# Optimization experiments

Hardware: AMD Instinct MI355X
Metric: run time of the kernel (lower is better)

Reference implementation:

```python
import jax, jax.numpy as jnp
import numpy as np

B, S, N, C = 8, 256, 256, 64
NH = 8
H, W = 256, 256
D = N * C // NH  # per-head channel dim = 2048
EPS = 1e-12


def window_reverse(windows, ws, Hh, Ww, Cc):
    # windows: (B, S, N, C) -> (B, H*W, C)
    b = windows.shape[0]
    x = windows.reshape(b, Hh // ws[0], Ww // ws[1], ws[0], ws[1], Cc)
    x = x.transpose(0, 1, 3, 2, 4, 5).reshape(b, Hh, Ww, Cc).reshape(b, Hh * Ww, Cc)
    return x


def window_partition(x, ws):
    # x: (B, H, W, C) -> (B, nWin, winElems, C)
    b, hh, ww, cc = x.shape
    x = x.reshape(b, hh // ws[0], ws[0], ww // ws[1], ws[1], cc)
    return x.transpose(0, 1, 3, 2, 4, 5).reshape(b, (hh // ws[0]) * (ww // ws[1]), ws[0] * ws[1], cc)


def setup_inputs() -> dict:
    key = jax.random.key(0)
    ks = jax.random.split(key, 6)
    x = jax.random.normal(ks[0], (B, S, N, C), dtype=jnp.float32)
    qkv_w = jax.random.normal(ks[1], (4 * C, C), dtype=jnp.float32) * 0.02
    qkv_b = jnp.zeros((4 * C,), dtype=jnp.float32)
    proj_w = jax.random.normal(ks[2], (C, C), dtype=jnp.float32) * 0.02
    proj_b = jnp.zeros((C,), dtype=jnp.float32)
    temperature1 = jnp.ones((NH, 1, 1), dtype=jnp.float32)
    temperature2 = jnp.ones((NH, 1, 1), dtype=jnp.float32)
    return {"x": x, "qkv_w": qkv_w, "qkv_b": qkv_b, "proj_w": proj_w,
            "proj_b": proj_b, "temperature1": temperature1, "temperature2": temperature2}


def reference(x, qkv_w, qkv_b, proj_w, proj_b, temperature1, temperature2):
    b, s, n, c = x.shape
    xf = x.reshape(b, s * n, c)
    # fused 4-way qkv projection (q, k, v_H, v_V)
    qkvv = (xf @ qkv_w.T + qkv_b).reshape(b, s, 4, NH, D).transpose(2, 0, 3, 1, 4)
    q, k, v_H, v_V = qkvv[0], qkvv[1], qkvv[2], qkvv[3]  # each (B, NH, S, D)

    # reorient v_V from H-windows (columns) to V-windows (rows)
    v_V = v_V.transpose(0, 2, 1, 3).reshape(b, s, n, c)       # (B,S,N,C)
    v_V = v_V.transpose(0, 2, 1, 3)                           # (B,N,S,C)
    v_V = window_reverse(v_V, (H, 1), H, W, c).reshape(b, H, W, c)
    v_V = window_partition(v_V, (1, W))                       # (B,H,W,C)
    v_V = v_V.transpose(0, 2, 1, 3)                           # (B,W,H,C) == (B,S,N,C)
    v_V = v_V.reshape(b, s, NH, D).transpose(0, 2, 1, 3)      # (B,NH,S,D)

    # cosine attention over S with per-head temperature
    qn = q / jnp.maximum(jnp.linalg.norm(q, axis=-1, keepdims=True), EPS)
    kn = k / jnp.maximum(jnp.linalg.norm(k, axis=-1, keepdims=True), EPS)
    sim = jnp.einsum('bhsd,bhtd->bhst', qn, kn)  # (B,NH,S,S)
    attn_H = jax.nn.softmax(sim * temperature1, axis=-1)
    attn_V = jax.nn.softmax(sim * temperature2, axis=-1)

    x_H = jnp.einsum('bhst,bhtd->bhsd', attn_H, v_H).transpose(0, 2, 1, 3).reshape(b, s * n, c)
    x_V = jnp.einsum('bhst,bhtd->bhsd', attn_V, v_V).transpose(0, 2, 1, 3).reshape(b, s * n, c)

    out = (x_H + x_V) @ proj_w.T + proj_b
    return out.reshape(b, s, n, c)
```

## Files before the change

kernel.cpp:

```cpp
#include <hip/hip_runtime.h>


using half_t = _Float16;
using half8 = __attribute__((ext_vector_type(8))) _Float16;
using f32x4 = __attribute__((ext_vector_type(4))) float;

#define NTOK 524288

#define GLDS(g, l) __builtin_amdgcn_global_load_lds( \
    (const __attribute__((address_space(1))) void*)(g), \
    (__attribute__((address_space(3))) void*)(l), 16, 0, 0)

#define WS_Q      0
#define WS_K      67108864
#define WS_VH     134217728
#define WS_VV     201326592
#define WS_XHV    268435456
#define WS_NQ     335544320
#define WS_NK     335609856
#define WS_WH     335675392
#define WS_WP     335708160

__global__ void kW0(const float* __restrict__ qkv_w, const float* __restrict__ proj_w,
                    half_t* __restrict__ Wh, half_t* __restrict__ Wp) {
    int tid = threadIdx.x;
    for (int i = tid; i < 256 * 64; i += 256) Wh[i] = (half_t)qkv_w[i];
    for (int i = tid; i < 64 * 64; i += 256) Wp[i] = (half_t)proj_w[i];
}

__device__ inline void y_tile_mfma(const float* __restrict__ xb,
                                   const half_t* __restrict__ Wh,
                                   int tbase, int hi, int lo,
                                   f32x4 (&acc)[4][4], int wave, int lane) {
    const int l15 = lane & 15, quad = lane >> 4;
#pragma unroll
    for (int kc = 0; kc < 2; ++kc) {
        const int c = kc * 32 + quad * 8;
        half8 afr[4];
#pragma unroll
        for (int mt = 0; mt < 4; ++mt) {
            int m = mt * 16 + l15;
            int token = tbase + (m >> 3) * hi + (m & 7) * lo;
            const float* p = xb + (size_t)token * 64 + c;
            f32x4 f0 = *(const f32x4*)p;
            f32x4 f1 = *(const f32x4*)(p + 4);
            half8 a;
            a[0] = (half_t)f0[0]; a[1] = (half_t)f0[1]; a[2] = (half_t)f0[2]; a[3] = (half_t)f0[3];
            a[4] = (half_t)f1[0]; a[5] = (half_t)f1[1]; a[6] = (half_t)f1[2]; a[7] = (half_t)f1[3];
            afr[mt] = a;
        }
#pragma unroll
        for (int i = 0; i < 4; ++i) {
            int j = (wave * 4 + i) * 16 + l15;
            half8 bfr = *(const half8*)(Wh + j * 64 + c);
#pragma unroll
            for (int mt = 0; mt < 4; ++mt)
                acc[mt][i] = __builtin_amdgcn_mfma_f32_16x16x32_f16(afr[mt], bfr, acc[mt][i], 0, 0, 0);
        }
    }
}

__device__ inline void y_dump_rowmajor(f32x4 (&acc)[4][4], const float* __restrict__ qkv_b,
                                       half_t* ylds, int wave, int lane) {
    const int l15 = lane & 15, quad = lane >> 4;
#pragma unroll
    for (int i = 0; i < 4; ++i) {
        int j = (wave * 4 + i) * 16 + l15;
        float bj = qkv_b[j];
#pragma unroll
        for (int mt = 0; mt < 4; ++mt)
#pragma unroll
            for (int r = 0; r < 4; ++r)
                ylds[(mt * 16 + quad * 4 + r) * 264 + j] = (half_t)(acc[mt][i][r] + bj);
    }
}

__device__ inline void y_dump_transposed(f32x4 (&acc)[4][4], const float* __restrict__ qkv_b,
                                         half_t* yldsT, int wave, int lane) {
    const int l15 = lane & 15, quad = lane >> 4;
#pragma unroll
    for (int i = 0; i < 4; ++i) {
        int j = (wave * 4 + i) * 16 + l15;
        float bj = qkv_b[j];
#pragma unroll
        for (int mt = 0; mt < 4; ++mt)
#pragma unroll
            for (int r = 0; r < 4; ++r)
                yldsT[j * 72 + mt * 16 + quad * 4 + r] = (half_t)(acc[mt][i][r] + bj);
    }
}

__global__ __launch_bounds__(256) void kA1(const float* __restrict__ x,
                                           const half_t* __restrict__ Wh,
                                           const float* __restrict__ qkv_b,
                                           half_t* __restrict__ Q, half_t* __restrict__ K,
                                           float* __restrict__ normQ, float* __restrict__ normK) {
    __shared__ half_t ylds[64 * 264];
    __shared__ float scr[256];
    int idx = blockIdx.x;
    int sb = idx & 31; idx >>= 5;
    int h = idx & 7; idx >>= 3;
    int g = idx & 1; int b = idx >> 1;
    int s0 = sb * 8;
    int n0 = g * 64 + h * 8;
    int tid = threadIdx.x, wave = tid >> 6, lane = tid & 63;
    const float* xb = x + (size_t)b * 65536 * 64;
    f32x4 acc[4][4];
#pragma unroll
    for (int a = 0; a < 4; ++a)
#pragma unroll
        for (int c = 0; c < 4; ++c) acc[a][c] = {0.f, 0.f, 0.f, 0.f};
    y_tile_mfma(xb, Wh, s0 * 256 + n0, 256, 1, acc, wave, lane);
    y_dump_rowmajor(acc, qkv_b, ylds, wave, lane);
    __syncthreads();
    half_t* dst = (g == 0 ? Q : K) + ((size_t)(b * 8 + h) * 256 + s0) * 2048;
    int ns = tid >> 5, jc = (tid & 31) * 8;
#pragma unroll
    for (int si = 0; si < 8; ++si) {
        half8 v = *(const half8*)&ylds[(si * 8 + ns) * 264 + jc];
        *(half8*)(dst + (size_t)si * 2048 + ns * 256 + jc) = v;
    }
    float sum = 0.f;
#pragma unroll
    for (int nn = 0; nn < 8; ++nn) {
        half8 v = *(const half8*)&ylds[((tid >> 5) * 8 + nn) * 264 + (tid & 31) * 8];
#pragma unroll
        for (int e = 0; e < 8; ++e) { float f = (float)v[e]; sum += f * f; }
    }
    scr[tid] = sum;
    __syncthreads();
    if (tid < 8) {
        float s = 0.f;
        for (int k2 = 0; k2 < 32; ++k2) s += scr[tid * 32 + k2];
        float* nd = (g == 0 ? normQ : normK);
        nd[(b * 8 + h) * 256 + s0 + tid] = s;
    }
}

__global__ __launch_bounds__(256) void kA2H(const float* __restrict__ x,
                                            const half_t* __restrict__ Wh,
                                            const float* __restrict__ qkv_b,
                                            half_t* __restrict__ VH) {
    __shared__ half_t yldsT[256 * 72];
    int idx = blockIdx.x;
    int sb = idx & 3; idx >>= 2;
    int nn = idx & 63; int b = idx >> 6;
    int h = nn >> 3, ns = nn & 7;
    int n = 128 + nn;
    int s0 = sb * 64;
    int tid = threadIdx.x, wave = tid >> 6, lane = tid & 63;
    const float* xb = x + (size_t)b * 65536 * 64;
    f32x4 acc[4][4];
#pragma unroll
    for (int a = 0; a < 4; ++a)
#pragma unroll
        for (int c = 0; c < 4; ++c) acc[a][c] = {0.f, 0.f, 0.f, 0.f};
    y_tile_mfma(xb, Wh, s0 * 256 + n, 2048, 256, acc, wave, lane);
    y_dump_transposed(acc, qkv_b, yldsT, wave, lane);
    __syncthreads();
    int jl = lane >> 3, tc = lane & 7;
    half_t* base = VH + ((size_t)(b * 8 + h) * 2048 + ns * 256) * 256 + s0 + tc * 8;
#pragma unroll
    for (int u = 0; u < 8; ++u) {
        int j = wave * 64 + u * 8 + jl;
        half8 v = *(const half8*)&yldsT[j * 72 + tc * 8];
        *(half8*)(base + (size_t)j * 256) = v;
    }
}

__global__ __launch_bounds__(256) void kA2V(const float* __restrict__ x,
                                            const half_t* __restrict__ Wh,
                                            const float* __restrict__ qkv_b,
                                            half_t* __restrict__ VV) {
    __shared__ half_t vlds[64 * 264];
    int idx = blockIdx.x;
    int st = idx & 255; int b = idx >> 8;
    int h = st >> 5;
    int tid = threadIdx.x, wave = tid >> 6, lane = tid & 63;
    const float* xb = x + (size_t)b * 65536 * 64;
    f32x4 acc[4][4];
#pragma unroll
    for (int a = 0; a < 4; ++a)
#pragma unroll
        for (int c = 0; c < 4; ++c) acc[a][c] = {0.f, 0.f, 0.f, 0.f};
    y_tile_mfma(xb, Wh, st * 256 + 192, 8, 1, acc, wave, lane);
    {
        const int l15 = lane & 15, quad = lane >> 4;
#pragma unroll
        for (int i = 0; i < 4; ++i) {
            int j = (wave * 4 + i) * 16 + l15;
            float bj = qkv_b[j];
            int dm = j & 63;
            int jc = j >> 6;
#pragma unroll
            for (int mt = 0; mt < 4; ++mt)
#pragma unroll
                for (int r = 0; r < 4; ++r) {
                    int m = mt * 16 + quad * 4 + r;
                    int t = 32 * (m >> 3) + 4 * (m & 7) + jc;
                    vlds[dm * 264 + t] = (half_t)(acc[mt][i][r] + bj);
                }
        }
    }
    __syncthreads();
    half_t* base = VV + ((size_t)(b * 8 + h) * 2048 + (st & 31) * 64) * 256;
    int l31 = lane & 31, lh = lane >> 5;
#pragma unroll
    for (int u = 0; u < 8; ++u) {
        int dm = u * 8 + wave * 2 + lh;
        half8 v = *(const half8*)&vlds[dm * 264 + l31 * 8];
        *(half8*)(base + (size_t)dm * 256 + l31 * 8) = v;
    }
}

__global__ __launch_bounds__(1024, 4) void kB(const half_t* __restrict__ Q, const half_t* __restrict__ K,
                                              const half_t* __restrict__ VH, const half_t* __restrict__ VV,
                                              const float* __restrict__ normQ, const float* __restrict__ normK,
                                              const float* __restrict__ temp1, const float* __restrict__ temp2,
                                              half_t* __restrict__ xhv) {
    extern __shared__ char smem[];
    char* Ks0 = smem;
    char* Ks1 = smem + 32768;
    char* Qs0 = smem + 65536;
    char* Qs1 = smem + 73728;
    half_t* PH = (half_t*)(smem + 81920);
    half_t* PV = (half_t*)(smem + 115712);
    float* rq  = (float*)(smem + 149504);
    float* rk  = (float*)(smem + 149760);

    int idx = blockIdx.x;
    int bh = idx & 63;
    int sqb = idx >> 6;
    int h = bh & 7, b = bh >> 3;
    int sq0 = sqb * 64;
    int tid = threadIdx.x, wave = tid >> 6, lane = tid & 63;
    int l15 = lane & 15, quad = lane >> 4;
    float t1 = temp1[h], t2 = temp2[h];
    const half_t* Qb = Q + (size_t)bh * 256 * 2048;
    const half_t* Kb = K + (size_t)bh * 256 * 2048;
    const half_t* VHb = VH + (size_t)bh * 2048 * 256;
    const half_t* VVb = VV + (size_t)bh * 2048 * 256;

    if (tid < 64) rq[tid] = 1.f / fmaxf(sqrtf(normQ[bh * 256 + sq0 + tid]), 1e-12f);
    if (tid < 256) rk[tid] = 1.f / fmaxf(sqrtf(normK[bh * 256 + tid]), 1e-12f);

    {
        const int l7 = lane & 7, l8 = lane >> 3;
        const int swzh = (l7 ^ (l8 & 7)) * 8;
        const half_t* gK0 = Kb + (size_t)(wave * 8 + l8) * 2048 + swzh;
        const half_t* gK1 = Kb + (size_t)(128 + wave * 8 + l8) * 2048 + swzh;
        const half_t* gQ  = Qb + (size_t)(sq0 + (wave & 7) * 8 + l8) * 2048 + swzh;

        auto STAGE = [&](int kk, char* KsB, char* QsB) {
            const int off = kk * 64;
            GLDS(gK0 + off, KsB + wave * 1024);
            GLDS(gK1 + off, KsB + 16384 + wave * 1024);
            if (wave < 8) GLDS(gQ + off, QsB + wave * 1024);
        };

        f32x4 acc1[4];
#pragma unroll
        for (int a = 0; a < 4; ++a) acc1[a] = {0.f, 0.f, 0.f, 0.f};
        const int tcol = wave * 16 + l15;
        const int ts7 = tcol & 7;

        auto COMPUTE = [&](const char* KsB_, const char* QsB_) {
            const half_t* KsB = (const half_t*)KsB_;
            const half_t* QsB = (const half_t*)QsB_;
#pragma unroll
            for (int sub = 0; sub < 2; ++sub) {
                int c16 = sub * 4 + quad;
                half8 bfr = *(const half8*)(KsB + tcol * 64 + (c16 ^ ts7) * 8);
#pragma unroll
                for (int mt = 0; mt < 4; ++mt) {
                    int m = mt * 16 + l15;
                    half8 afr = *(const half8*)(QsB + m * 64 + (c16 ^ (m & 7)) * 8);
                    acc1[mt] = __builtin_amdgcn_mfma_f32_16x16x32_f16(afr, bfr, acc1[mt], 0, 0, 0);
                }
            }
        };

        STAGE(0, Ks0, Qs0);
        __syncthreads();
        for (int kk = 0; kk < 32; kk += 2) {
            if (kk + 1 < 32) STAGE(kk + 1, Ks1, Qs1);
            COMPUTE(Ks0, Qs0);
            __syncthreads();
            if (kk + 2 < 32) STAGE(kk + 2, Ks0, Qs0);
            COMPUTE(Ks1, Qs1);
            __syncthreads();
        }
        float rkt = rk[tcol];
#pragma unroll
        for (int mt = 0; mt < 4; ++mt)
#pragma unroll
            for (int r = 0; r < 4; ++r) {
                int row = mt * 16 + quad * 4 + r;
                PH[row * 264 + tcol] = (half_t)(acc1[mt][r] * rq[row] * rkt);
            }
    }
    __syncthreads();

    {
        int r_ = tid >> 4, cc = tid & 15;
        half_t* phrow = &PH[r_ * 264 + cc * 16];
        half_t* pvrow = &PV[r_ * 264 + cc * 16];
        half8 v0 = *(const half8*)phrow;
        half8 v1 = *(const half8*)(phrow + 8);
        float fv[16];
#pragma unroll
        for (int e = 0; e < 8; ++e) { fv[e] = (float)v0[e]; fv[8 + e] = (float)v1[e]; }
        float mx = fv[0], mn = fv[0];
#pragma unroll
        for (int e = 1; e < 16; ++e) { mx = fmaxf(mx, fv[e]); mn = fminf(mn, fv[e]); }
#pragma unroll
        for (int m = 1; m < 16; m <<= 1) {
            mx = fmaxf(mx, __shfl_xor(mx, m, 16));
            mn = fminf(mn, __shfl_xor(mn, m, 16));
        }
        float mh = (t1 >= 0.f) ? t1 * mx : t1 * mn;
        float mv = (t2 >= 0.f) ? t2 * mx : t2 * mn;
        float sh = 0.f, sv = 0.f;
#pragma unroll
        for (int e = 0; e < 16; ++e) {
            sh += __expf(fv[e] * t1 - mh);
            sv += __expf(fv[e] * t2 - mv);
        }
#pragma unroll
        for (int m = 1; m < 16; m <<= 1) {
            sh += __shfl_xor(sh, m, 16);
            sv += __shfl_xor(sv, m, 16);
        }
        float rh = 1.f / sh, rv = 1.f / sv;
        half8 o0, o1, p0, p1;
#pragma unroll
        for (int e = 0; e < 8; ++e) {
            o0[e] = (half_t)(__expf(fv[e] * t1 - mh) * rh);
            o1[e] = (half_t)(__expf(fv[8 + e] * t1 - mh) * rh);
            p0[e] = (half_t)(__expf(fv[e] * t2 - mv) * rv);
            p1[e] = (half_t)(__expf(fv[8 + e] * t2 - mv) * rv);
        }
        *(half8*)phrow = o0; *(half8*)(phrow + 8) = o1;
        *(half8*)pvrow = p0; *(half8*)(pvrow + 8) = p1;
    }
    __syncthreads();

    const int rr = lane >> 3, c8 = (lane & 7) * 8;
#pragma unroll
    for (int i2 = 0; i2 < 2; ++i2) {
        int d0 = wave * 64 + i2 * 1024;
        f32x4 acc2[4][4];
#pragma unroll
        for (int a = 0; a < 4; ++a)
#pragma unroll
            for (int c = 0; c < 4; ++c) acc2[a][c] = {0.f, 0.f, 0.f, 0.f};
        for (int kc = 0; kc < 8; ++kc) {
            int tk = kc * 32 + quad * 8;
            half8 afr[4];
#pragma unroll
            for (int mt = 0; mt < 4; ++mt)
                afr[mt] = *(const half8*)&PH[(mt * 16 + l15) * 264 + tk];
#pragma unroll
            for (int nt = 0; nt < 4; ++nt) {
                half8 bfr = *(const half8*)(VHb + (size_t)(d0 + nt * 16 + l15) * 256 + tk);
#pragma unroll
                for (int mt = 0; mt < 4; ++mt)
                    acc2[mt][nt] = __builtin_amdgcn_mfma_f32_16x16x32_f16(afr[mt], bfr, acc2[mt][nt], 0, 0, 0);
            }
#pragma unroll
            for (int mt = 0; mt < 4; ++mt)
                afr[mt] = *(const half8*)&PV[(mt * 16 + l15) * 264 + tk];
#pragma unroll
            for (int nt = 0; nt < 4; ++nt) {
                half8 bfr = *(const half8*)(VVb + (size_t)(d0 + nt * 16 + l15) * 256 + tk);
#pragma unroll
                for (int mt = 0; mt < 4; ++mt)
                    acc2[mt][nt] = __builtin_amdgcn_mfma_f32_16x16x32_f16(afr[mt], bfr, acc2[mt][nt], 0, 0, 0);
            }
        }
        int db = wave + i2 * 16;
        half_t* xbase = xhv + (((size_t)(b * 8 + h) * 32 + db) * 256 + sq0) * 64;
#pragma unroll
        for (int mt = 0; mt < 4; ++mt) {
            half_t* myscr = (half_t*)(smem + wave * 5120 + (mt & 1) * 2560);
#pragma unroll
            for (int nt = 0; nt < 4; ++nt)
#pragma unroll
                for (int r = 0; r < 4; ++r)
                    myscr[(quad * 4 + r) * 72 + nt * 16 + l15] = (half_t)acc2[mt][nt][r];
#pragma unroll
            for (int u = 0; u < 2; ++u) {
                half8 v = *(const half8*)&myscr[(u * 8 + rr) * 72 + c8];
                *(half8*)(xbase + (size_t)(mt * 16 + u * 8 + rr) * 64 + c8) = v;
            }
        }
    }
}

__global__ __launch_bounds__(256) void kC(const half_t* __restrict__ xhv, const half_t* __restrict__ Wp,
                                          const float* __restrict__ proj_b, float* __restrict__ out) {
    __shared__ float ot[64 * 68];
    int tid = threadIdx.x, wave = tid >> 6, lane = tid & 63;
    int l15 = lane & 15, quad = lane >> 4;
    size_t T0 = (size_t)blockIdx.x * 64;
    int b = (int)(T0 >> 16);
    int s = (int)((T0 >> 8) & 255);
    int n0 = (int)(T0 & 255);
    f32x4 acc[4];
#pragma unroll
    for (int a = 0; a < 4; ++a) acc[a] = {0.f, 0.f, 0.f, 0.f};
#pragma unroll
    for (int kc = 0; kc < 2; ++kc) {
        int c = kc * 32 + quad * 8;
        half8 bfr = *(const half8*)(Wp + (wave * 16 + l15) * 64 + c);
#pragma unroll
        for (int mt = 0; mt < 4; ++mt) {
            int n = n0 + mt * 16 + l15;
            int hh = n >> 5, db = n & 31;
            const half_t* arow = xhv + (((size_t)(b * 8 + hh) * 32 + db) * 256 + s) * 64;
            half8 afr = *(const half8*)(arow + c);
            acc[mt] = __builtin_amdgcn_mfma_f32_16x16x32_f16(afr, bfr, acc[mt], 0, 0, 0);
        }
    }
    float bj = proj_b[wave * 16 + l15];
#pragma unroll
    for (int mt = 0; mt < 4; ++mt)
#pragma unroll
        for (int r = 0; r < 4; ++r)
            ot[(mt * 16 + quad * 4 + r) * 68 + wave * 16 + l15] = acc[mt][r] + bj;
    __syncthreads();
    int row = tid >> 2;
#pragma unroll
    for (int u = 0; u < 4; ++u) {
        int col = (tid & 3) * 4 + u * 16;
        f32x4 v = *(const f32x4*)&ot[row * 68 + col];
        *(f32x4*)(out + (T0 + row) * 64 + col) = v;
    }
}

extern "C" void kernel_launch(void* const* d_in, const int* in_sizes, int n_in,
                              void* d_out, int out_size, void* d_ws, size_t ws_size,
                              hipStream_t stream) {
    const float* x      = (const float*)d_in[0];
    const float* qkv_w  = (const float*)d_in[1];
    const float* qkv_b  = (const float*)d_in[2];
    const float* proj_w = (const float*)d_in[3];
    const float* proj_b = (const float*)d_in[4];
    const float* temp1  = (const float*)d_in[5];
    const float* temp2  = (const float*)d_in[6];
    char* ws = (char*)d_ws;
    half_t* Q   = (half_t*)(ws + WS_Q);
    half_t* K   = (half_t*)(ws + WS_K);
    half_t* VH  = (half_t*)(ws + WS_VH);
    half_t* VV  = (half_t*)(ws + WS_VV);
    half_t* xhv = (half_t*)(ws + WS_XHV);
    float* normQ = (float*)(ws + WS_NQ);
    float* normK = (float*)(ws + WS_NK);
    half_t* Wh  = (half_t*)(ws + WS_WH);
    half_t* Wp  = (half_t*)(ws + WS_WP);
    float* out = (float*)d_out;

    hipFuncSetAttribute((const void*)kB, hipFuncAttributeMaxDynamicSharedMemorySize, 150784);

    kW0<<<1, 256, 0, stream>>>(qkv_w, proj_w, Wh, Wp);
    kA1<<<4096, 256, 0, stream>>>(x, Wh, qkv_b, Q, K, normQ, normK);
    kA2H<<<2048, 256, 0, stream>>>(x, Wh, qkv_b, VH);
    kA2V<<<2048, 256, 0, stream>>>(x, Wh, qkv_b, VV);
    kB<<<256, 1024, 150784, stream>>>(Q, K, VH, VV, normQ, normK, temp1, temp2, xhv);
    kC<<<8192, 256, 0, stream>>>(xhv, Wp, proj_b, out);
}
```

Before: 590.8 us.

## Triple-buffer QK staging in attention kernel and vectorize LDS epilogue stores

Result: no change. 586.3 us (-0.8%).

```diff
diff --git a/kernel.cpp b/kernel.cpp
--- a/kernel.cpp
+++ b/kernel.cpp
@@ -2,6 +2,7 @@
 
 
 using half_t = _Float16;
+using half4 = __attribute__((ext_vector_type(4))) _Float16;
 using half8 = __attribute__((ext_vector_type(8))) _Float16;
 using f32x4 = __attribute__((ext_vector_type(4))) float;
 
@@ -60,18 +61,35 @@
     }
 }
 
-__device__ inline void y_dump_rowmajor(f32x4 (&acc)[4][4], const float* __restrict__ qkv_b,
-                                       half_t* ylds, int wave, int lane) {
+__device__ inline void y_tile_mfma_swapped(const float* __restrict__ xb,
+                                           const half_t* __restrict__ Wh,
+                                           int tbase, int hi, int lo,
+                                           f32x4 (&acc)[4][4], int wave, int lane) {
     const int l15 = lane & 15, quad = lane >> 4;
 #pragma unroll
-    for (int i = 0; i < 4; ++i) {
-        int j = (wave * 4 + i) * 16 + l15;
-        float bj = qkv_b[j];
-#pragma unroll
-        for (int mt = 0; mt < 4; ++mt)
-#pragma unroll
-            for (int r = 0; r < 4; ++r)
-                ylds[(mt * 16 + quad * 4 + r) * 264 + j] = (half_t)(acc[mt][i][r] + bj);
+    for (int kc = 0; kc < 2; ++kc) {
+        const int c = kc * 32 + quad * 8;
+        half8 bx[4];
+#pragma unroll
+        for (int mt = 0; mt < 4; ++mt) {
+            int m = mt * 16 + l15;
+            int token = tbase + (m >> 3) * hi + (m & 7) * lo;
+            const float* p = xb + (size_t)token * 64 + c;
+            f32x4 f0 = *(const f32x4*)p;
+            f32x4 f1 = *(const f32x4*)(p + 4);
+            half8 a;
+            a[0] = (half_t)f0[0]; a[1] = (half_t)f0[1]; a[2] = (half_t)f0[2]; a[3] = (half_t)f0[3];
+            a[4] = (half_t)f1[0]; a[5] = (half_t)f1[1]; a[6] = (half_t)f1[2]; a[7] = (half_t)f1[3];
+            bx[mt] = a;
+        }
+#pragma unroll
+        for (int i = 0; i < 4; ++i) {
+            int j = (wave * 4 + i) * 16 + l15;
+            half8 aw = *(const half8*)(Wh + j * 64 + c);
+#pragma unroll
+            for (int mt = 0; mt < 4; ++mt)
+                acc[i][mt] = __builtin_amdgcn_mfma_f32_16x16x32_f16(aw, bx[mt], acc[i][mt], 0, 0, 0);
+        }
     }
 }
 
@@ -104,14 +122,27 @@
     int s0 = sb * 8;
     int n0 = g * 64 + h * 8;
     int tid = threadIdx.x, wave = tid >> 6, lane = tid & 63;
+    const int l15 = lane & 15, quad = lane >> 4;
     const float* xb = x + (size_t)b * 65536 * 64;
     f32x4 acc[4][4];
 #pragma unroll
     for (int a = 0; a < 4; ++a)
 #pragma unroll
         for (int c = 0; c < 4; ++c) acc[a][c] = {0.f, 0.f, 0.f, 0.f};
-    y_tile_mfma(xb, Wh, s0 * 256 + n0, 256, 1, acc, wave, lane);
-    y_dump_rowmajor(acc, qkv_b, ylds, wave, lane);
+    y_tile_mfma_swapped(xb, Wh, s0 * 256 + n0, 256, 1, acc, wave, lane);
+#pragma unroll
+    for (int i = 0; i < 4; ++i) {
+        int j0 = (wave * 4 + i) * 16 + quad * 4;
+        f32x4 bj = *(const f32x4*)&qkv_b[j0];
+#pragma unroll
+        for (int mt = 0; mt < 4; ++mt) {
+            int m = mt * 16 + l15;
+            half4 v;
+#pragma unroll
+            for (int r = 0; r < 4; ++r) v[r] = (half_t)(acc[i][mt][r] + bj[r]);
+            *(half4*)&ylds[m * 264 + j0] = v;
+        }
+    }
     __syncthreads();
     half_t* dst = (g == 0 ? Q : K) + ((size_t)(b * 8 + h) * 256 + s0) * 2048;
     int ns = tid >> 5, jc = (tid & 31) * 8;
@@ -149,6 +180,7 @@
     int n = 128 + nn;
     int s0 = sb * 64;
     int tid = threadIdx.x, wave = tid >> 6, lane = tid & 63;
+    const int l15 = lane & 15, quad = lane >> 4;
     const float* xb = x + (size_t)b * 65536 * 64;
     f32x4 acc[4][4];
 #pragma unroll
@@ -156,7 +188,18 @@
 #pragma unroll
         for (int c = 0; c < 4; ++c) acc[a][c] = {0.f, 0.f, 0.f, 0.f};
     y_tile_mfma(xb, Wh, s0 * 256 + n, 2048, 256, acc, wave, lane);
-    y_dump_transposed(acc, qkv_b, yldsT, wave, lane);
+#pragma unroll
+    for (int i = 0; i < 4; ++i) {
+        int j = (wave * 4 + i) * 16 + l15;
+        float bj = qkv_b[j];
+#pragma unroll
+        for (int mt = 0; mt < 4; ++mt) {
+            half4 v;
+#pragma unroll
+            for (int r = 0; r < 4; ++r) v[r] = (half_t)(acc[mt][i][r] + bj);
+            *(half4*)&yldsT[j * 72 + mt * 16 + quad * 4] = v;
+        }
+    }
     __syncthreads();
     int jl = lane >> 3, tc = lane & 7;
     half_t* base = VH + ((size_t)(b * 8 + h) * 2048 + ns * 256) * 256 + s0 + tc * 8;
@@ -219,14 +262,10 @@
                                               const float* __restrict__ temp1, const float* __restrict__ temp2,
                                               half_t* __restrict__ xhv) {
     extern __shared__ char smem[];
-    char* Ks0 = smem;
-    char* Ks1 = smem + 32768;
-    char* Qs0 = smem + 65536;
-    char* Qs1 = smem + 73728;
-    half_t* PH = (half_t*)(smem + 81920);
-    half_t* PV = (half_t*)(smem + 115712);
-    float* rq  = (float*)(smem + 149504);
-    float* rk  = (float*)(smem + 149760);
+    half_t* PH = (half_t*)smem;
+    half_t* PV = (half_t*)(smem + 40960);
+    float* rq  = (float*)(smem + 122880);
+    float* rk  = (float*)(smem + 123136);
 
     int idx = blockIdx.x;
     int bh = idx & 63;
@@ -251,11 +290,11 @@
         const half_t* gK1 = Kb + (size_t)(128 + wave * 8 + l8) * 2048 + swzh;
         const half_t* gQ  = Qb + (size_t)(sq0 + (wave & 7) * 8 + l8) * 2048 + swzh;
 
-        auto STAGE = [&](int kk, char* KsB, char* QsB) {
+        auto STAGE = [&](int kk, char* B) {
             const int off = kk * 64;
-            GLDS(gK0 + off, KsB + wave * 1024);
-            GLDS(gK1 + off, KsB + 16384 + wave * 1024);
-            if (wave < 8) GLDS(gQ + off, QsB + wave * 1024);
+            GLDS(gK0 + off, B + wave * 1024);
+            GLDS(gK1 + off, B + 16384 + wave * 1024);
+            if (wave < 8) GLDS(gQ + off, B + 32768 + wave * 1024);
         };
 
         f32x4 acc1[4];
@@ -264,9 +303,9 @@
         const int tcol = wave * 16 + l15;
         const int ts7 = tcol & 7;
 
-        auto COMPUTE = [&](const char* KsB_, const char* QsB_) {
-            const half_t* KsB = (const half_t*)KsB_;
-            const half_t* QsB = (const half_t*)QsB_;
+        auto COMPUTE = [&](const char* B) {
+            const half_t* KsB = (const half_t*)B;
+            const half_t* QsB = (const half_t*)(B + 32768);
 #pragma unroll
             for (int sub = 0; sub < 2; ++sub) {
                 int c16 = sub * 4 + quad;
@@ -280,16 +319,26 @@
             }
         };
 
-        STAGE(0, Ks0, Qs0);
+        STAGE(0, smem);
+        STAGE(1, smem + 40960);
         __syncthreads();
-        for (int kk = 0; kk < 32; kk += 2) {
-            if (kk + 1 < 32) STAGE(kk + 1, Ks1, Qs1);
-            COMPUTE(Ks0, Qs0);
-            __syncthreads();
-            if (kk + 2 < 32) STAGE(kk + 2, Ks0, Qs0);
-            COMPUTE(Ks1, Qs1);
-            __syncthreads();
-        }
+        int c0 = 0, c2 = 2;
+        for (int kk = 0; kk < 30; ++kk) {
+            COMPUTE(smem + c0 * 40960);
+            STAGE(kk + 2, smem + c2 * 40960);
+            if (wave < 8) { asm volatile("s_waitcnt vmcnt(3)" ::: "memory"); }
+            else          { asm volatile("s_waitcnt vmcnt(2)" ::: "memory"); }
+            __builtin_amdgcn_s_barrier();
+            __builtin_amdgcn_sched_barrier(0);
+            c0 = (c0 == 2) ? 0 : c0 + 1;
+            c2 = (c2 == 2) ? 0 : c2 + 1;
+        }
+        COMPUTE(smem + c0 * 40960);
+        asm volatile("s_waitcnt vmcnt(0)" ::: "memory");
+        __builtin_amdgcn_s_barrier();
+        __builtin_amdgcn_sched_barrier(0);
+        c0 = (c0 == 2) ? 0 : c0 + 1;
+        COMPUTE(smem + c0 * 40960);
         float rkt = rk[tcol];
 #pragma unroll
         for (int mt = 0; mt < 4; ++mt)
@@ -346,6 +395,7 @@
     __syncthreads();
 
     const int rr = lane >> 3, c8 = (lane & 7) * 8;
+    half_t* myscr = (half_t*)(smem + 81920 + wave * 2560);
 #pragma unroll
     for (int i2 = 0; i2 < 2; ++i2) {
         int d0 = wave * 64 + i2 * 1024;
@@ -382,7 +432,6 @@
         half_t* xbase = xhv + (((size_t)(b * 8 + h) * 32 + db) * 256 + sq0) * 64;
 #pragma unroll
         for (int mt = 0; mt < 4; ++mt) {
-            half_t* myscr = (half_t*)(smem + wave * 5120 + (mt & 1) * 2560);
 #pragma unroll
             for (int nt = 0; nt < 4; ++nt)
 #pragma unroll
@@ -460,12 +509,12 @@
     half_t* Wp  = (half_t*)(ws + WS_WP);
     float* out = (float*)d_out;
 
-    hipFuncSetAttribute((const void*)kB, hipFuncAttributeMaxDynamicSharedMemorySize, 150784);
+    hipFuncSetAttribute((const void*)kB, hipFuncAttributeMaxDynamicSharedMemorySize, 124160);
 
     kW0<<<1, 256, 0, stream>>>(qkv_w, proj_w, Wh, Wp);
     kA1<<<4096, 256, 0, stream>>>(x, Wh, qkv_b, Q, K, normQ, normK);
     kA2H<<<2048, 256, 0, stream>>>(x, Wh, qkv_b, VH);
     kA2V<<<2048, 256, 0, stream>>>(x, Wh, qkv_b, VV);
-    kB<<<256, 1024, 150784, stream>>>(Q, K, VH, VV, normQ, normK, temp1, temp2, xhv);
+    kB<<<256, 1024, 124160, stream>>>(Q, K, VH, VV, normQ, normK, temp1, temp2, xhv);
     kC<<<8192, 256, 0, stream>>>(xhv, Wp, proj_b, out);
 }
```
